# Kernel tuning notes

Measured on AMD Instinct MI355X. Metric: run time of the kernel, lower is better.

The kernel has to match this reference:

```python
import jax, jax.numpy as jnp
import numpy as np

NUM_LAYERS = 4
UNITS = 512
DX = 8e-6
WAVELENGTHS = np.array([4.5e-7, 5.32e-7, 6.33e-7], dtype=np.float32)
Z_LAYERS = 0.03
Z_PROP = 0.05
NUM_MODES = 16
BASE_IDX = 1  # base_wavelength_idx in source


def setup_inputs() -> dict:
    key = jax.random.key(0)
    k1, k2 = jax.random.split(key)
    C = len(WAVELENGTHS)
    x = jax.random.normal(k1, (NUM_MODES, C, UNITS, UNITS), dtype=jnp.float32)
    # phase = rand(units, units) * pi, one per layer
    phases = jax.random.uniform(k2, (NUM_LAYERS, UNITS, UNITS), dtype=jnp.float32) * np.pi
    # wavelength_coefficients initialized to base_wavelength / wl (learned params)
    base = WAVELENGTHS[BASE_IDX]
    coeffs = jnp.tile(jnp.asarray(base / WAVELENGTHS, dtype=jnp.float32), (NUM_LAYERS, 1))
    lams = jnp.asarray(WAVELENGTHS)
    return {"x": x, "phases": phases, "coeffs": coeffs, "lams": lams}


def _transfer_fn(lams, z, n, dx):
    # Band-limited angular-spectrum transfer function, per wavelength: [C, H, W]
    f = jnp.fft.fftfreq(n, d=dx).astype(jnp.float32)
    fx2 = f[None, :] ** 2 + f[:, None] ** 2          # [H, W]
    arg = (1.0 / lams)[:, None, None] ** 2 - fx2[None]  # [C, H, W]
    valid = arg > 0
    kz = 2.0 * jnp.pi * jnp.sqrt(jnp.where(valid, arg, 0.0))
    return jnp.where(valid, jnp.exp(1j * (kz * z).astype(jnp.float32)), 0.0)


def _propagate(field, Hf):
    # field: [B, C, H, W] complex; Hf: [C, H, W] — batched angular-spectrum step
    return jnp.fft.ifft2(jnp.fft.fft2(field) * Hf[None])


def reference(x, phases, coeffs, lams):
    n = x.shape[-1]
    H_layer = _transfer_fn(lams, Z_LAYERS, n, DX)  # inter-layer propagation
    H_final = _transfer_fn(lams, Z_PROP, n, DX)    # propagation to detector
    field = x.astype(jnp.complex64)
    for l in range(NUM_LAYERS):
        # per-wavelength effective phase: phase * coeff (depth_factor == 1)
        eff = phases[l][None, :, :] * coeffs[l][:, None, None]  # [C, H, W]
        field = field * jnp.exp(1j * eff)[None]
        field = _propagate(field, H_layer)
    field = _propagate(field, H_final)
    return jnp.abs(field) ** 2
```

## Files before the change

### kernel.cpp

```cpp
#include <hip/hip_runtime.h>
#include <hip/hip_fp16.h>
#include <math.h>


#define TWOPI_F 6.2831854820251465f
#define RSQ2    0.70710678f
#define NPIX    (48*512*512)

__device__ __forceinline__ float2 cadd(float2 a, float2 b){ return make_float2(a.x+b.x, a.y+b.y); }
__device__ __forceinline__ float2 csub(float2 a, float2 b){ return make_float2(a.x-b.x, a.y-b.y); }
__device__ __forceinline__ float2 cmul(float2 a, float2 b){ return make_float2(a.x*b.x - a.y*b.y, a.x*b.y + a.y*b.x); }

template<int S> __device__ __forceinline__ float2 mul_i(float2 a){
  return (S>0) ? make_float2(-a.y, a.x) : make_float2(a.y, -a.x);
}
template<int S> __device__ __forceinline__ float2 mul_w1(float2 a){
  return (S>0) ? make_float2(RSQ2*(a.x-a.y), RSQ2*(a.x+a.y))
               : make_float2(RSQ2*(a.x+a.y), RSQ2*(a.y-a.x));
}
template<int S> __device__ __forceinline__ float2 mul_w3(float2 a){
  return (S>0) ? make_float2(RSQ2*(-a.x-a.y), RSQ2*(a.x-a.y))
               : make_float2(RSQ2*(a.y-a.x), RSQ2*(-a.x-a.y));
}
template<int S> __device__ __forceinline__ float2 cmul_tw(float2 v, float2 w){
  float wy = (S>0) ? -w.y : w.y;
  return make_float2(v.x*w.x - v.y*wy, v.x*wy + v.y*w.x);
}

__device__ __forceinline__ float4 f4add(float4 a, float4 b){ return make_float4(a.x+b.x,a.y+b.y,a.z+b.z,a.w+b.w); }
__device__ __forceinline__ float4 f4sub(float4 a, float4 b){ return make_float4(a.x-b.x,a.y-b.y,a.z-b.z,a.w-b.w); }
template<int S> __device__ __forceinline__ float4 mul_i4(float4 a){
  return (S>0) ? make_float4(-a.y,a.x,-a.w,a.z) : make_float4(a.y,-a.x,a.w,-a.z);
}
template<int S> __device__ __forceinline__ float4 mul_w14(float4 a){
  return (S>0) ? make_float4(RSQ2*(a.x-a.y), RSQ2*(a.x+a.y), RSQ2*(a.z-a.w), RSQ2*(a.z+a.w))
               : make_float4(RSQ2*(a.x+a.y), RSQ2*(a.y-a.x), RSQ2*(a.z+a.w), RSQ2*(a.w-a.z));
}
template<int S> __device__ __forceinline__ float4 mul_w34(float4 a){
  return (S>0) ? make_float4(RSQ2*(-a.x-a.y), RSQ2*(a.x-a.y), RSQ2*(-a.z-a.w), RSQ2*(a.z-a.w))
               : make_float4(RSQ2*(a.y-a.x), RSQ2*(-a.x-a.y), RSQ2*(a.w-a.z), RSQ2*(-a.z-a.w));
}
template<int S> __device__ __forceinline__ float4 cmul_tw4(float4 v, float2 w){
  float wy = (S>0) ? -w.y : w.y;
  return make_float4(v.x*w.x - v.y*wy, v.x*wy + v.y*w.x,
                     v.z*w.x - v.w*wy, v.z*wy + v.w*w.x);
}
__device__ __forceinline__ float4 cmulh4(float4 v, float4 h){
  return make_float4(v.x*h.x - v.y*h.y, v.x*h.y + v.y*h.x,
                     v.z*h.z - v.w*h.w, v.z*h.w + v.w*h.z);
}

template<int S>
__device__ __forceinline__ void dft8(const float2* a, float2* d){
  float2 b0=cadd(a[0],a[4]), b1=cadd(a[1],a[5]), b2=cadd(a[2],a[6]), b3=cadd(a[3],a[7]);
  float2 b4=csub(a[0],a[4]);
  float2 b5=mul_w1<S>(csub(a[1],a[5]));
  float2 b6=mul_i<S> (csub(a[2],a[6]));
  float2 b7=mul_w3<S>(csub(a[3],a[7]));
  float2 c0=cadd(b0,b2), c2=csub(b0,b2);
  float2 c1=cadd(b1,b3), c3=mul_i<S>(csub(b1,b3));
  float2 c4=cadd(b4,b6), c6=csub(b4,b6);
  float2 c5=cadd(b5,b7), c7=mul_i<S>(csub(b5,b7));
  d[0]=cadd(c0,c1); d[1]=csub(c0,c1);
  d[2]=cadd(c2,c3); d[3]=csub(c2,c3);
  d[4]=cadd(c4,c5); d[5]=csub(c4,c5);
  d[6]=cadd(c6,c7); d[7]=csub(c6,c7);
}
template<int S>
__device__ __forceinline__ void dft8_4(const float4* a, float4* d){
  float4 b0=f4add(a[0],a[4]), b1=f4add(a[1],a[5]), b2=f4add(a[2],a[6]), b3=f4add(a[3],a[7]);
  float4 b4=f4sub(a[0],a[4]);
  float4 b5=mul_w14<S>(f4sub(a[1],a[5]));
  float4 b6=mul_i4<S> (f4sub(a[2],a[6]));
  float4 b7=mul_w34<S>(f4sub(a[3],a[7]));
  float4 c0=f4add(b0,b2), c2=f4sub(b0,b2);
  float4 c1=f4add(b1,b3), c3=mul_i4<S>(f4sub(b1,b3));
  float4 c4=f4add(b4,b6), c6=f4sub(b4,b6);
  float4 c5=f4add(b5,b7), c7=mul_i4<S>(f4sub(b5,b7));
  d[0]=f4add(c0,c1); d[1]=f4sub(c0,c1);
  d[2]=f4add(c2,c3); d[3]=f4sub(c2,c3);
  d[4]=f4add(c4,c5); d[5]=f4sub(c4,c5);
  d[6]=f4add(c6,c7); d[7]=f4sub(c6,c7);
}

__device__ __forceinline__ int SWZR(int i){ return i ^ ((i>>4)&7); }
__device__ __forceinline__ int CSWZ(int e, int cx){ return (e<<3) + (cx ^ ((e>>3)&7)); }

__device__ __forceinline__ void lds_fence(){ asm volatile("s_waitcnt lgkmcnt(0)" ::: "memory"); }

__device__ __forceinline__ void make_tw(int t, float2* tw0, float2* tw1){
  float sn, cs;
  __sincosf((TWOPI_F/512.0f)*(float)t, &sn, &cs);
  float2 w0 = make_float2(cs, -sn);
  tw0[0] = make_float2(1.0f, 0.0f);
  #pragma unroll
  for(int k=1;k<8;k++) tw0[k] = cmul(tw0[k-1], w0);
  int p = t>>3;
  __sincosf((TWOPI_F/64.0f)*(float)p, &sn, &cs);
  float2 w1 = make_float2(cs, -sn);
  tw1[0] = make_float2(1.0f, 0.0f);
  #pragma unroll
  for(int k=1;k<8;k++) tw1[k] = cmul(tw1[k-1], w1);
}

template<int S>
__device__ __forceinline__ void fft512_wv(float2* a, float2* o, float2* B, int t,
                                          float scale, const float2* tw0, const float2* tw1){
  const int km[8] = {0,4,2,6,1,5,3,7};
  float2 d[8];
  dft8<S>(a, d);
  #pragma unroll
  for(int k=0;k<8;k++)
    B[SWZR(8*t+k)] = (k==0) ? d[0] : cmul_tw<S>(d[km[k]], tw0[k]);
  lds_fence();
  #pragma unroll
  for(int r=0;r<8;r++) a[r] = B[SWZR(t+64*r)];
  lds_fence();
  dft8<S>(a, d);
  {
    int p = t>>3, q = t&7;
    #pragma unroll
    for(int k=0;k<8;k++)
      B[SWZR(q + 64*p + 8*k)] = (k==0) ? d[0] : cmul_tw<S>(d[km[k]], tw1[k]);
  }
  lds_fence();
  #pragma unroll
  for(int r=0;r<8;r++) a[r] = B[SWZR(t+64*r)];
  lds_fence();
  dft8<S>(a, d);
  #pragma unroll
  for(int k=0;k<8;k++) o[k] = make_float2(d[km[k]].x*scale, d[km[k]].y*scale);
}

template<int S>
__device__ __forceinline__ void fft512_pr(float4* a, float4* o, float4* B, int t, int cx,
                                          float scale, const float2* tw0, const float2* tw1){
  const int km[8] = {0,4,2,6,1,5,3,7};
  float4 d[8];
  dft8_4<S>(a, d);
  #pragma unroll
  for(int k=0;k<8;k++)
    B[CSWZ(8*t+k, cx)] = (k==0) ? d[0] : cmul_tw4<S>(d[km[k]], tw0[k]);
  __syncthreads();
  #pragma unroll
  for(int r=0;r<8;r++) a[r] = B[CSWZ(t+64*r, cx)];
  __syncthreads();
  dft8_4<S>(a, d);
  {
    int p = t>>3, q = t&7;
    #pragma unroll
    for(int k=0;k<8;k++)
      B[CSWZ(q + 64*p + 8*k, cx)] = (k==0) ? d[0] : cmul_tw4<S>(d[km[k]], tw1[k]);
  }
  __syncthreads();
  #pragma unroll
  for(int r=0;r<8;r++) a[r] = B[CSWZ(t+64*r, cx)];
  dft8_4<S>(a, d);
  #pragma unroll
  for(int k=0;k<8;k++)
    o[k] = make_float4(d[km[k]].x*scale, d[km[k]].y*scale, d[km[k]].z*scale, d[km[k]].w*scale);
}

template<int S, int LD>
__device__ __forceinline__ void fft512_1b(float2* a, float2* o, float2* B, int t,
                                          float scale, const float2* tw0, const float2* tw1){
  const int km[8] = {0,4,2,6,1,5,3,7};
  float2 d[8];
  dft8<S>(a, d);
  #pragma unroll
  for(int k=0;k<8;k++)
    B[(8*t+k)*LD] = (k==0) ? d[0] : cmul_tw<S>(d[km[k]], tw0[k]);
  __syncthreads();
  #pragma unroll
  for(int r=0;r<8;r++) a[r] = B[(t+64*r)*LD];
  __syncthreads();
  dft8<S>(a, d);
  {
    int p = t>>3, q = t&7;
    #pragma unroll
    for(int k=0;k<8;k++)
      B[(q + 64*p + 8*k)*LD] = (k==0) ? d[0] : cmul_tw<S>(d[km[k]], tw1[k]);
  }
  __syncthreads();
  #pragma unroll
  for(int r=0;r<8;r++) a[r] = B[(t+64*r)*LD];
  dft8<S>(a, d);
  #pragma unroll
  for(int k=0;k<8;k++) o[k] = make_float2(d[km[k]].x*scale, d[km[k]].y*scale);
}


struct AccH {
  __half2* p;
  __device__ __forceinline__ float2 ld(int i) const { return __half22float2(p[i]); }
  __device__ __forceinline__ void   st(int i, float2 v) const { p[i] = __floats2half2_rn(v.x, v.y); }
};
struct AccS {
  float* re; float* im;
  __device__ __forceinline__ float2 ld(int i) const { return make_float2(re[i], im[i]); }
  __device__ __forceinline__ void   st(int i, float2 v) const { re[i]=v.x; im[i]=v.y; }
};


__device__ __forceinline__ float2 phase_of(float kz, float zf){
  float tt = __fmul_rn(kz, zf);
  double dt = (double)tt;
  double q  = rint(dt * 0.15915494309189535);
  double rr = fma(-q, 6.283185307179586, dt);
  float sn, cs; __sincosf((float)rr, &sn, &cs);
  return make_float2(cs, sn);
}

__global__ __launch_bounds__(256) void k_htab(const float* __restrict__ lams,
                                              float2* __restrict__ H1, float2* __restrict__ H12){
  int e = blockIdx.x*256 + threadIdx.x;
  int c = e >> 18, fy = (e>>9)&511, col = e&511;
  const float lam = lams[c];
  const float il  = 1.0f / lam;
  const float il2 = __fmul_rn(il, il);
  const float DEN = (float)(512.0 * 8e-6);
  int   sx  = (col < 256) ? col : col - 512;
  int   sy  = (fy  < 256) ? fy  : fy  - 512;
  float fxv = (float)sx / DEN, fyv = (float)sy / DEN;
  float arg = __fsub_rn(il2, __fadd_rn(__fmul_rn(fxv,fxv), __fmul_rn(fyv,fyv)));
  float2 h1 = make_float2(0.0f,0.0f), h12 = h1;
  if(arg > 0.0f){
    float s  = (float)sqrt((double)arg);
    float kz = __fmul_rn(6.2831854820251465f, s);
    h1  = phase_of(kz, 0.03f);
    h12 = cmul(h1, phase_of(kz, 0.05f));
  }
  H1[e] = h1; H12[e] = h12;
}


template<class Acc>
__global__ __launch_bounds__(256) void k_row_first(
    const float* __restrict__ x, Acc f,
    const float* __restrict__ phases, const float* __restrict__ coeffs)
{
  __shared__ float2 lds[4][512];
  const int w = threadIdx.x >> 6, t = threadIdx.x & 63;
  const int img = blockIdx.x, c = img % 3;
  const int row = (blockIdx.y<<2) + w;
  const int base = (img*512 + row)*512;
  const float* ph = phases + row*512;
  const float coeff = coeffs[c];
  float2 tw0[8], tw1[8]; make_tw(t, tw0, tw1);
  float2 a[8], o[8];
  #pragma unroll
  for(int r=0;r<8;r++){
    int i = t + (r<<6);
    float xv = x[base+i];
    float th = __fmul_rn(ph[i], coeff);
    float sn, cs; __sincosf(th, &sn, &cs);
    a[r] = make_float2(xv*cs, xv*sn);
  }
  fft512_wv<-1>(a, o, lds[w], t, 1.0f, tw0, tw1);
  #pragma unroll
  for(int k=0;k<8;k++){ int i=t+(k<<6); f.st(base+i, o[k]); }
}

template<class Acc>
__global__ __launch_bounds__(256) void k_row_mid(
    Acc f, const float* __restrict__ phases, const float* __restrict__ coeffs, int layer)
{
  __shared__ float2 lds[4][512];
  const int w = threadIdx.x >> 6, t = threadIdx.x & 63;
  const int img = blockIdx.x, c = img % 3;
  const int row = (blockIdx.y<<2) + w;
  const int base = (img*512 + row)*512;
  const float* ph = phases + (layer*512 + row)*512;
  const float coeff = coeffs[layer*3 + c];
  float2 tw0[8], tw1[8]; make_tw(t, tw0, tw1);
  float2 a[8], o[8], pv[8];
  #pragma unroll
  for(int r=0;r<8;r++){
    int i=t+(r<<6); a[r]=f.ld(base+i);
    float th = __fmul_rn(ph[i], coeff);
    float sn, cs; __sincosf(th, &sn, &cs);
    pv[r] = make_float2(cs, sn);
  }
  fft512_wv<+1>(a, o, lds[w], t, 1.0f/512.0f, tw0, tw1);
  #pragma unroll
  for(int k=0;k<8;k++) a[k] = cmul(o[k], pv[k]);
  fft512_wv<-1>(a, o, lds[w], t, 1.0f, tw0, tw1);
  #pragma unroll
  for(int k=0;k<8;k++){ int i=t+(k<<6); f.st(base+i, o[k]); }
}

template<class Acc>
__global__ __launch_bounds__(256) void k_row_last(
    Acc f, float* __restrict__ out)
{
  __shared__ float2 lds[4][512];
  const int w = threadIdx.x >> 6, t = threadIdx.x & 63;
  const int img = blockIdx.x;
  const int row = (blockIdx.y<<2) + w;
  const int base = (img*512 + row)*512;
  float2 tw0[8], tw1[8]; make_tw(t, tw0, tw1);
  float2 a[8], o[8];
  #pragma unroll
  for(int r=0;r<8;r++){ int i=t+(r<<6); a[r]=f.ld(base+i); }
  fft512_wv<+1>(a, o, lds[w], t, 1.0f/512.0f, tw0, tw1);
  #pragma unroll
  for(int k=0;k<8;k++){ int i=t+(k<<6); out[base+i] = o[k].x*o[k].x + o[k].y*o[k].y; }
}


__global__ __launch_bounds__(512, 2) void k_colp(
    __half2* __restrict__ F, const float2* __restrict__ Htab)
{
  __shared__ float4 lds[512*8];
  const int cx = threadIdx.x & 7, t = threadIdx.x >> 3;
  const int img = blockIdx.x, c = img % 3;
  const int col = (blockIdx.y<<4) + (cx<<1);
  const int ibase = (img<<18) + col;
  float2 tw0[8], tw1[8]; make_tw(t, tw0, tw1);
  float4 a[8], o[8], h[8];
  #pragma unroll
  for(int r=0;r<8;r++){
    int gi = ibase + ((t+(r<<6))<<9);
    uint2 raw = *reinterpret_cast<const uint2*>(F + gi);
    __half2 v0, v1;
    *reinterpret_cast<unsigned int*>(&v0) = raw.x;
    *reinterpret_cast<unsigned int*>(&v1) = raw.y;
    float2 fA = __half22float2(v0), fB = __half22float2(v1);
    a[r] = make_float4(fA.x, fA.y, fB.x, fB.y);
  }
  #pragma unroll
  for(int k=0;k<8;k++){
    int fy = t + (k<<6);
    h[k] = *reinterpret_cast<const float4*>(Htab + (c<<18) + (fy<<9) + col);
  }
  fft512_pr<-1>(a, o, lds, t, cx, 1.0f, tw0, tw1);
  #pragma unroll
  for(int k=0;k<8;k++) a[k] = cmulh4(o[k], h[k]);
  __syncthreads();
  fft512_pr<+1>(a, o, lds, t, cx, 1.0f/512.0f, tw0, tw1);
  #pragma unroll
  for(int k=0;k<8;k++){
    int gi = ibase + ((t+(k<<6))<<9);
    __half2 v0 = __floats2half2_rn(o[k].x, o[k].y);
    __half2 v1 = __floats2half2_rn(o[k].z, o[k].w);
    uint2 raw;
    raw.x = *reinterpret_cast<unsigned int*>(&v0);
    raw.y = *reinterpret_cast<unsigned int*>(&v1);
    *reinterpret_cast<uint2*>(F + gi) = raw;
  }
}


template<class Acc, bool TAB>
__global__ __launch_bounds__(512, 2) void k_col8(
    Acc f, const float2* __restrict__ Htab, const float* __restrict__ lams, float z1, float z2)
{
  __shared__ float2 lds[512][9];
  const int cx = threadIdx.x & 7, t = threadIdx.x >> 3;
  const int img = blockIdx.x, c = img % 3;
  const int col = (blockIdx.y<<3) + cx;
  const int ibase = (img<<18) + col;
  float2 tw0[8], tw1[8]; make_tw(t, tw0, tw1);
  float2 a[8], o[8], h[8];
  #pragma unroll
  for(int r=0;r<8;r++){ int gi = ibase + ((t+(r<<6))<<9); a[r]=f.ld(gi); }
  if(TAB){
    const float2* Hrow = Htab + (c<<18) + col;
    #pragma unroll
    for(int k=0;k<8;k++) h[k] = Hrow[(t+(k<<6))<<9];
  } else {
    const float lam = lams[c];
    const float il  = 1.0f / lam;
    const float il2 = __fmul_rn(il, il);
    const float DEN = (float)(512.0 * 8e-6);
    int   sx  = (col < 256) ? col : col - 512;
    float fxv = (float)sx / DEN;
    float fx2 = __fmul_rn(fxv, fxv);
    #pragma unroll
    for(int k=0;k<8;k++){
      int fy = t + (k<<6);
      int sy = (fy < 256) ? fy : fy - 512;
      float fyv = (float)sy / DEN;
      float arg = __fsub_rn(il2, __fadd_rn(fx2, __fmul_rn(fyv,fyv)));
      h[k] = make_float2(0.0f, 0.0f);
      if(arg > 0.0f){
        float s  = (float)sqrt((double)arg);
        float kz = __fmul_rn(6.2831854820251465f, s);
        h[k] = phase_of(kz, z1);
        if(z2 != 0.0f) h[k] = cmul(h[k], phase_of(kz, z2));
      }
    }
  }
  fft512_1b<-1,9>(a, o, &lds[0][cx], t, 1.0f, tw0, tw1);
  #pragma unroll
  for(int k=0;k<8;k++) a[k] = cmul(o[k], h[k]);
  __syncthreads();
  fft512_1b<+1,9>(a, o, &lds[0][cx], t, 1.0f/512.0f, tw0, tw1);
  #pragma unroll
  for(int k=0;k<8;k++){ int gi = ibase + ((t+(k<<6))<<9); f.st(gi, o[k]); }
}


extern "C" void kernel_launch(void* const* d_in, const int* in_sizes, int n_in,
                              void* d_out, int out_size, void* d_ws, size_t ws_size,
                              hipStream_t stream)
{
  const float* x      = (const float*)d_in[0];
  const float* phases = (const float*)d_in[1];
  const float* coeffs = (const float*)d_in[2];
  const float* lams   = (const float*)d_in[3];
  float* out = (float*)d_out;

  const size_t fldH = (size_t)NPIX*4;
  const size_t splB = (size_t)NPIX*4;
  const size_t tabB = (size_t)3*512*512*8;

  dim3 gA(48,128), bA(256);
  dim3 gP(48,32),  bP(512);
  dim3 gB(48,64),  bB(512);
  dim3 gH(3*512*512/256), bH(256);

  if(ws_size >= fldH + 2*tabB){
    AccH f { (__half2*)d_ws };
    float2* H1  = (float2*)((char*)d_ws + fldH);
    float2* H12 = H1 + 3*512*512;
    k_htab<<<gH, bH, 0, stream>>>(lams, H1, H12);
    k_row_first<AccH><<<gA, bA, 0, stream>>>(x, f, phases, coeffs);
    for(int l=1; l<=3; l++){
      k_colp<<<gP, bP, 0, stream>>>((__half2*)d_ws, H1);
      k_row_mid<AccH><<<gA, bA, 0, stream>>>(f, phases, coeffs, l);
    }
    k_colp<<<gP, bP, 0, stream>>>((__half2*)d_ws, H12);
    k_row_last<AccH><<<gA, bA, 0, stream>>>(f, out);
  } else if(ws_size >= splB + 2*tabB){
    AccS f { out, (float*)d_ws };
    float2* H1  = (float2*)((char*)d_ws + splB);
    float2* H12 = H1 + 3*512*512;
    k_htab<<<gH, bH, 0, stream>>>(lams, H1, H12);
    k_row_first<AccS><<<gA, bA, 0, stream>>>(x, f, phases, coeffs);
    for(int l=1; l<=3; l++){
      k_col8<AccS,true><<<gB, bB, 0, stream>>>(f, H1, lams, 0.03f, 0.0f);
      k_row_mid<AccS><<<gA, bA, 0, stream>>>(f, phases, coeffs, l);
    }
    k_col8<AccS,true><<<gB, bB, 0, stream>>>(f, H12, lams, 0.03f, 0.0f);
    k_row_last<AccS><<<gA, bA, 0, stream>>>(f, out);
  } else {
    AccS f { out, (float*)d_ws };
    k_row_first<AccS><<<gA, bA, 0, stream>>>(x, f, phases, coeffs);
    for(int l=1; l<=3; l++){
      k_col8<AccS,false><<<gB, bB, 0, stream>>>(f, nullptr, lams, 0.03f, 0.0f);
      k_row_mid<AccS><<<gA, bA, 0, stream>>>(f, phases, coeffs, l);
    }
    k_col8<AccS,false><<<gB, bB, 0, stream>>>(f, nullptr, lams, 0.03f, 0.05f);
    k_row_last<AccS><<<gA, bA, 0, stream>>>(f, out);
  }
}
```

Before: 296.7 us.

## Pack column-FFT LDS exchange in fp16 and compute twiddles on the fly for higher occupancy

The column-pass kernel now stores its LDS transpose buffer as packed half2 pairs, which halves shared memory per block from 64KB to 32KB. Twiddle tables are no longer held in registers; each stage builds its twiddles from one sincos followed by repeated complex multiplies. The transfer-function values are kept packed in fp16 registers. Launch bounds rise from 2 to 3 blocks per CU to exploit the lower LDS and register use. This adds fp16 rounding at the intermediate FFT stages and for the H coefficients, and the recursive twiddle products accumulate error.

Result: slower. 423.4 us (+42.7%).

```diff
diff --git a/kernel.cpp b/kernel.cpp
--- a/kernel.cpp
+++ b/kernel.cpp
@@ -48,6 +48,22 @@
 __device__ __forceinline__ float4 cmulh4(float4 v, float4 h){
   return make_float4(v.x*h.x - v.y*h.y, v.x*h.y + v.y*h.x,
                      v.z*h.z - v.w*h.w, v.z*h.w + v.w*h.z);
+}
+
+__device__ __forceinline__ uint2 pk4(float4 v){
+  __half2 h0 = __floats2half2_rn(v.x, v.y);
+  __half2 h1 = __floats2half2_rn(v.z, v.w);
+  uint2 u;
+  u.x = *reinterpret_cast<unsigned int*>(&h0);
+  u.y = *reinterpret_cast<unsigned int*>(&h1);
+  return u;
+}
+__device__ __forceinline__ float4 upk4(uint2 u){
+  __half2 h0, h1;
+  *reinterpret_cast<unsigned int*>(&h0) = u.x;
+  *reinterpret_cast<unsigned int*>(&h1) = u.y;
+  float2 a = __half22float2(h0), b = __half22float2(h1);
+  return make_float4(a.x, a.y, b.x, b.y);
 }
 
 template<int S>
@@ -133,28 +149,42 @@
 }
 
 template<int S>
-__device__ __forceinline__ void fft512_pr(float4* a, float4* o, float4* B, int t, int cx,
-                                          float scale, const float2* tw0, const float2* tw1){
+__device__ __forceinline__ void fft512_ph(float4* a, float4* o, uint2* B, int t, int cx,
+                                          float scale){
   const int km[8] = {0,4,2,6,1,5,3,7};
   float4 d[8];
   dft8_4<S>(a, d);
-  #pragma unroll
-  for(int k=0;k<8;k++)
-    B[CSWZ(8*t+k, cx)] = (k==0) ? d[0] : cmul_tw4<S>(d[km[k]], tw0[k]);
-  __syncthreads();
-  #pragma unroll
-  for(int r=0;r<8;r++) a[r] = B[CSWZ(t+64*r, cx)];
+  {
+    float sn, cs; __sincosf((TWOPI_F/512.0f)*(float)t, &sn, &cs);
+    float2 w0 = make_float2(cs, -sn);
+    float2 tw = make_float2(1.0f, 0.0f);
+    #pragma unroll
+    for(int k=0;k<8;k++){
+      float4 v = (k==0) ? d[0] : cmul_tw4<S>(d[km[k]], tw);
+      B[CSWZ(8*t+k, cx)] = pk4(v);
+      tw = cmul(tw, w0);
+    }
+  }
+  __syncthreads();
+  #pragma unroll
+  for(int r=0;r<8;r++) a[r] = upk4(B[CSWZ(t+64*r, cx)]);
   __syncthreads();
   dft8_4<S>(a, d);
   {
     int p = t>>3, q = t&7;
-    #pragma unroll
-    for(int k=0;k<8;k++)
-      B[CSWZ(q + 64*p + 8*k, cx)] = (k==0) ? d[0] : cmul_tw4<S>(d[km[k]], tw1[k]);
-  }
-  __syncthreads();
-  #pragma unroll
-  for(int r=0;r<8;r++) a[r] = B[CSWZ(t+64*r, cx)];
+    float sn, cs; __sincosf((TWOPI_F/64.0f)*(float)p, &sn, &cs);
+    float2 w1 = make_float2(cs, -sn);
+    float2 tw = make_float2(1.0f, 0.0f);
+    #pragma unroll
+    for(int k=0;k<8;k++){
+      float4 v = (k==0) ? d[0] : cmul_tw4<S>(d[km[k]], tw);
+      B[CSWZ(q + 64*p + 8*k, cx)] = pk4(v);
+      tw = cmul(tw, w1);
+    }
+  }
+  __syncthreads();
+  #pragma unroll
+  for(int r=0;r<8;r++) a[r] = upk4(B[CSWZ(t+64*r, cx)]);
   dft8_4<S>(a, d);
   #pragma unroll
   for(int k=0;k<8;k++)
@@ -308,45 +338,37 @@
 }
 
 
-__global__ __launch_bounds__(512, 2) void k_colp(
+__global__ __launch_bounds__(512, 3) void k_colf(
     __half2* __restrict__ F, const float2* __restrict__ Htab)
 {
-  __shared__ float4 lds[512*8];
+  __shared__ uint2 lds[512*8];
   const int cx = threadIdx.x & 7, t = threadIdx.x >> 3;
   const int img = blockIdx.x, c = img % 3;
   const int col = (blockIdx.y<<4) + (cx<<1);
   const int ibase = (img<<18) + col;
-  float2 tw0[8], tw1[8]; make_tw(t, tw0, tw1);
-  float4 a[8], o[8], h[8];
+  float4 a[8], o[8];
+  uint2 hp[8];
   #pragma unroll
   for(int r=0;r<8;r++){
     int gi = ibase + ((t+(r<<6))<<9);
     uint2 raw = *reinterpret_cast<const uint2*>(F + gi);
-    __half2 v0, v1;
-    *reinterpret_cast<unsigned int*>(&v0) = raw.x;
-    *reinterpret_cast<unsigned int*>(&v1) = raw.y;
-    float2 fA = __half22float2(v0), fB = __half22float2(v1);
-    a[r] = make_float4(fA.x, fA.y, fB.x, fB.y);
+    a[r] = upk4(raw);
   }
   #pragma unroll
   for(int k=0;k<8;k++){
     int fy = t + (k<<6);
-    h[k] = *reinterpret_cast<const float4*>(Htab + (c<<18) + (fy<<9) + col);
-  }
-  fft512_pr<-1>(a, o, lds, t, cx, 1.0f, tw0, tw1);
-  #pragma unroll
-  for(int k=0;k<8;k++) a[k] = cmulh4(o[k], h[k]);
-  __syncthreads();
-  fft512_pr<+1>(a, o, lds, t, cx, 1.0f/512.0f, tw0, tw1);
+    float4 hv = *reinterpret_cast<const float4*>(Htab + (c<<18) + (fy<<9) + col);
+    hp[k] = pk4(hv);
+  }
+  fft512_ph<-1>(a, o, lds, t, cx, 1.0f);
+  #pragma unroll
+  for(int k=0;k<8;k++) a[k] = cmulh4(o[k], upk4(hp[k]));
+  __syncthreads();
+  fft512_ph<+1>(a, o, lds, t, cx, 1.0f/512.0f);
   #pragma unroll
   for(int k=0;k<8;k++){
     int gi = ibase + ((t+(k<<6))<<9);
-    __half2 v0 = __floats2half2_rn(o[k].x, o[k].y);
-    __half2 v1 = __floats2half2_rn(o[k].z, o[k].w);
-    uint2 raw;
-    raw.x = *reinterpret_cast<unsigned int*>(&v0);
-    raw.y = *reinterpret_cast<unsigned int*>(&v1);
-    *reinterpret_cast<uint2*>(F + gi) = raw;
+    *reinterpret_cast<uint2*>(F + gi) = pk4(o[k]);
   }
 }
 
@@ -427,10 +449,10 @@
     k_htab<<<gH, bH, 0, stream>>>(lams, H1, H12);
     k_row_first<AccH><<<gA, bA, 0, stream>>>(x, f, phases, coeffs);
     for(int l=1; l<=3; l++){
-      k_colp<<<gP, bP, 0, stream>>>((__half2*)d_ws, H1);
+      k_colf<<<gP, bP, 0, stream>>>((__half2*)d_ws, H1);
       k_row_mid<AccH><<<gA, bA, 0, stream>>>(f, phases, coeffs, l);
     }
-    k_colp<<<gP, bP, 0, stream>>>((__half2*)d_ws, H12);
+    k_colf<<<gP, bP, 0, stream>>>((__half2*)d_ws, H12);
     k_row_last<AccH><<<gA, bA, 0, stream>>>(f, out);
   } else if(ws_size >= splB + 2*tabB){
     AccS f { out, (float*)d_ws };
```
